# Performance work log

Measured on AMD Instinct MI355X. Metric: run time of the kernel, lower is better.

The kernel has to match this reference:

```python
import jax, jax.numpy as jnp
import numpy as np

DIM = 192
NUM_HEADS = 4
B, H, W = 2, 256, 256
EPS = 1e-12  # torch F.normalize default eps


def setup_inputs() -> dict:
    key = jax.random.key(0)
    k1, k2, k3 = jax.random.split(key, 3)
    x = jax.random.normal(k1, (B, DIM, H, W), dtype=jnp.float32)
    # depthwise qkv conv: groups=DIM, each group maps 1 in-ch -> 3 out-ch; torch OIHW layout (3*DIM, 1, 3, 3)
    w_qkv = jax.random.normal(k2, (3 * DIM, 1, 3, 3), dtype=jnp.float32) * 0.1
    temperature = jnp.ones((NUM_HEADS, 1, 1), dtype=jnp.float32)
    # 1x1 projection conv, stored as [out, in]
    w_proj = jax.random.normal(k3, (DIM, DIM), dtype=jnp.float32) * (1.0 / np.sqrt(DIM))
    return {"x": x, "w_qkv": w_qkv, "temperature": temperature, "w_proj": w_proj}


def reference(x, w_qkv, temperature, w_proj):
    b, c, h, w = x.shape
    num_heads = temperature.shape[0]
    ch = c // num_heads  # channels per head
    # grouped (depthwise) 3x3 conv producing qkv; torch grouped-conv channel order
    # matches feature_group_count ordering (3 consecutive out-chs per group)... but
    # note torch chunk(3, dim=1) splits the 3*c output into contiguous thirds, so
    # q gets out-channels [0, c), etc. We replicate exactly with same layout.
    qkv = jax.lax.conv_general_dilated(
        x, w_qkv, window_strides=(1, 1), padding=((1, 1), (1, 1)),
        feature_group_count=c,
        dimension_numbers=("NCHW", "OIHW", "NCHW"))
    q, k, v = jnp.split(qkv, 3, axis=1)  # each [b, c, h, w]
    q = q.reshape(b, num_heads, ch, h * w)
    k = k.reshape(b, num_heads, ch, h * w)
    v = v.reshape(b, num_heads, ch, h * w)
    # L2 normalize along spatial dim (torch F.normalize with eps clamp)
    q = q / jnp.maximum(jnp.linalg.norm(q, axis=-1, keepdims=True), EPS)
    k = k / jnp.maximum(jnp.linalg.norm(k, axis=-1, keepdims=True), EPS)
    # channel-channel cosine attention, [b, head, ch, ch] (small)
    attn = jnp.einsum("bhcn,bhdn->bhcd", q, k) * temperature
    attn = jax.nn.softmax(attn, axis=-1)
    out = jnp.einsum("bhcd,bhdn->bhcn", attn, v).reshape(b, c, h, w)
    # 1x1 projection conv
    out = jnp.einsum("oi,bihw->bohw", w_proj, out)
    return out
```

## Files before the change

kernel.cpp:

```cpp
#include <hip/hip_runtime.h>
#include <math.h>

#define BB 2
#define CC 192
#define NH 4
#define CH 48
#define SRCP 16
#define HH 256
#define WW 256
#define NPIX (HH*WW)

typedef __attribute__((ext_vector_type(8))) short short8;
typedef __attribute__((ext_vector_type(4))) float f4;

static __device__ __forceinline__ unsigned short f2bf(float f) {
    union { float f; unsigned int u; } c; c.f = f;
    unsigned int r = c.u + 0x7fffu + ((c.u >> 16) & 1u);
    return (unsigned short)(r >> 16);
}

__global__ __launch_bounds__(256, 3) void k_conv(
    const float* __restrict__ x, const float* __restrict__ wqkv,
    unsigned short* __restrict__ vws, float* __restrict__ Sws,
    float* __restrict__ sqws)
{
    __shared__ unsigned int qk32[2][CH][132];

    const int tid = threadIdx.x;
    const int hd = blockIdx.x;
    const int y  = blockIdx.y;
    const int b  = blockIdx.z;

    {
        const int xp = tid;
        const int y0 = (y > 0) ? (y-1) : 0;
        const int y2 = (y < HH-1) ? (y+1) : y;
        const int xl = (xp > 0) ? (xp-1) : 0;
        const int xr = (xp < WW-1) ? (xp+1) : xp;
        const float my0 = (y > 0) ? 1.f : 0.f;
        const float my2 = (y < HH-1) ? 1.f : 0.f;
        const float mx0 = (xp > 0) ? 1.f : 0.f;
        const float mx2 = (xp < WW-1) ? 1.f : 0.f;
        const float m00 = my0*mx0, m02 = my0*mx2, m20 = my2*mx0, m22 = my2*mx2;

        #pragma unroll
        for (int type = 0; type < 2; ++type) {
            const int srcbase = type*64 + SRCP*hd;
            const float* wt = wqkv + type*(CC*9) + hd*(CH*9);
            for (int g4 = 0; g4 < SRCP; g4 += 4) {
                float A[4][9];
                #pragma unroll
                for (int u = 0; u < 4; ++u) {
                    const float* base = x + ((size_t)(b*CC + srcbase + g4 + u)*HH)*WW;
                    const float* r0 = base + (size_t)y0*WW;
                    const float* r1 = base + (size_t)y *WW;
                    const float* r2 = base + (size_t)y2*WW;
                    A[u][0] = r0[xl]; A[u][1] = r0[xp]; A[u][2] = r0[xr];
                    A[u][3] = r1[xl]; A[u][4] = r1[xp]; A[u][5] = r1[xr];
                    A[u][6] = r2[xl]; A[u][7] = r2[xp]; A[u][8] = r2[xr];
                }
                #pragma unroll
                for (int u = 0; u < 4; ++u) {
                    const int g = g4 + u;
                    float a00 = A[u][0]*m00, a01 = A[u][1]*my0, a02 = A[u][2]*m02;
                    float a10 = A[u][3]*mx0, a11 = A[u][4],     a12 = A[u][5]*mx2;
                    float a20 = A[u][6]*m20, a21 = A[u][7]*my2, a22 = A[u][8]*m22;
                    #pragma unroll
                    for (int r = 0; r < 3; ++r) {
                        const int cl = 3*g + r;
                        const float* w = wt + cl*9;
                        float val = a00*w[0] + a01*w[1] + a02*w[2]
                                  + a10*w[3] + a11*w[4] + a12*w[5]
                                  + a20*w[6] + a21*w[7] + a22*w[8];
                        ((unsigned short*)&qk32[type][cl][0])[xp] = f2bf(val);
                    }
                }
            }
        }

        unsigned int vpack[24];
        {
            const int srcbase = 128 + SRCP*hd;
            const float* wt = wqkv + 2*(CC*9) + hd*(CH*9);
            #pragma unroll
            for (int g4 = 0; g4 < SRCP; g4 += 4) {
                float A[4][9];
                #pragma unroll
                for (int u = 0; u < 4; ++u) {
                    const float* base = x + ((size_t)(b*CC + srcbase + g4 + u)*HH)*WW;
                    const float* r0 = base + (size_t)y0*WW;
                    const float* r1 = base + (size_t)y *WW;
                    const float* r2 = base + (size_t)y2*WW;
                    A[u][0] = r0[xl]; A[u][1] = r0[xp]; A[u][2] = r0[xr];
                    A[u][3] = r1[xl]; A[u][4] = r1[xp]; A[u][5] = r1[xr];
                    A[u][6] = r2[xl]; A[u][7] = r2[xp]; A[u][8] = r2[xr];
                }
                #pragma unroll
                for (int u = 0; u < 4; ++u) {
                    const int g = g4 + u;
                    float a00 = A[u][0]*m00, a01 = A[u][1]*my0, a02 = A[u][2]*m02;
                    float a10 = A[u][3]*mx0, a11 = A[u][4],     a12 = A[u][5]*mx2;
                    float a20 = A[u][6]*m20, a21 = A[u][7]*my2, a22 = A[u][8]*m22;
                    #pragma unroll
                    for (int r = 0; r < 3; ++r) {
                        const int cl = 3*g + r;
                        const float* w = wt + cl*9;
                        float val = a00*w[0] + a01*w[1] + a02*w[2]
                                  + a10*w[3] + a11*w[4] + a12*w[5]
                                  + a20*w[6] + a21*w[7] + a22*w[8];
                        unsigned int uu = f2bf(val);
                        if (cl & 1) vpack[cl >> 1] |= (uu << 16);
                        else        vpack[cl >> 1]  = uu;
                    }
                }
            }
        }
        {
            unsigned short* vp = vws + ((size_t)b*NPIX + (size_t)y*WW + xp)*CC + hd*CH;
            #pragma unroll
            for (int st = 0; st < 6; ++st) {
                uint4 u; u.x = vpack[st*4+0]; u.y = vpack[st*4+1];
                         u.z = vpack[st*4+2]; u.w = vpack[st*4+3];
                *(uint4*)(vp + st*8) = u;
            }
        }
    }
    __syncthreads();

    if (tid < 2*CH) {
        const int which = tid / CH;
        const int cl = tid - which*CH;
        const uint4* row = (const uint4*)&qk32[which][cl][0];
        float ssum = 0.f;
        for (int j = 0; j < 32; ++j) {
            uint4 u = row[j];
            #pragma unroll
            for (int q4 = 0; q4 < 4; ++q4) {
                unsigned int w = (&u.x)[q4];
                float lo = __uint_as_float(w << 16);
                float hi = __uint_as_float(w & 0xffff0000u);
                ssum = fmaf(lo, lo, ssum);
                ssum = fmaf(hi, hi, ssum);
            }
        }
        atomicAdd(&sqws[((b*NH + hd)*2 + which)*CH + cl], ssum);
    }

    {
        const int lane = tid & 63;
        const int wv = tid >> 6;
        const int m = lane & 15, quad = lane >> 4;
        for (int p = wv; p < 9; p += 4) {
            const int ct = p / 3, dt = p - ct*3;
            f4 acc = {0.f, 0.f, 0.f, 0.f};
            const char* qbase = (const char*)&qk32[0][ct*16 + m][0] + quad*16;
            const char* kbase = (const char*)&qk32[1][dt*16 + m][0] + quad*16;
            #pragma unroll
            for (int ks = 0; ks < 8; ++ks) {
                short8 afr = *(const short8*)(qbase + ks*64);
                short8 bfr = *(const short8*)(kbase + ks*64);
                acc = __builtin_amdgcn_mfma_f32_16x16x32_bf16(afr, bfr, acc, 0, 0, 0);
            }
            const int c0 = ct*16 + quad*4, d = dt*16 + m;
            float* Sp = Sws + ((size_t)(b*NH + hd)*CH + c0)*CH + d;
            #pragma unroll
            for (int r = 0; r < 4; ++r) atomicAdd(Sp + r*CH, acc[r]);
        }
    }
}

__global__ __launch_bounds__(256) void k_attn(
    const float* __restrict__ Sws, const float* __restrict__ sqws,
    const float* __restrict__ temp, const float* __restrict__ wproj,
    unsigned short* __restrict__ W2bf)
{
    __shared__ float att[CH][CH+1];
    __shared__ float wp[CC][CH+1];
    __shared__ float nrm[2][CH];

    const int tid = threadIdx.x;
    const int b  = blockIdx.x >> 2;
    const int hd = blockIdx.x & 3;

    if (tid < 2*CH) {
        int which = tid / CH, cl = tid - which*CH;
        nrm[which][cl] = fmaxf(sqrtf(sqws[((b*NH + hd)*2 + which)*CH + cl]), 1e-12f);
    }
    __syncthreads();

    const float tscale = temp[hd];
    for (int m = tid; m < CH*CH; m += 256) {
        int c = m / CH, d = m - c*CH;
        att[c][d] = Sws[((size_t)(b*NH + hd)*CH + c)*CH + d] * tscale
                    / (nrm[0][c] * nrm[1][d]);
    }
    __syncthreads();

    if (tid < CH) {
        float mx = -1e30f;
        for (int d = 0; d < CH; ++d) mx = fmaxf(mx, att[tid][d]);
        float sm = 0.f;
        for (int d = 0; d < CH; ++d) { float e = expf(att[tid][d] - mx); att[tid][d] = e; sm += e; }
        float inv = 1.f / sm;
        for (int d = 0; d < CH; ++d) att[tid][d] *= inv;
    }

    for (int m = tid; m < CC*CH; m += 256) {
        int o = m / CH, il = m - o*CH;
        wp[o][il] = wproj[o*CC + hd*CH + il];
    }
    __syncthreads();

    const int o0  = (tid & 31) * 6;
    const int dl0 = (tid >> 5) * 6;
    float a[6][6];
    #pragma unroll
    for (int i = 0; i < 6; ++i)
        #pragma unroll
        for (int j = 0; j < 6; ++j) a[i][j] = 0.f;
    for (int il = 0; il < CH; ++il) {
        float wv[6], av[6];
        #pragma unroll
        for (int i = 0; i < 6; ++i) wv[i] = wp[o0+i][il];
        #pragma unroll
        for (int j = 0; j < 6; ++j) av[j] = att[il][dl0+j];
        #pragma unroll
        for (int i = 0; i < 6; ++i)
            #pragma unroll
            for (int j = 0; j < 6; ++j)
                a[i][j] = fmaf(wv[i], av[j], a[i][j]);
    }
    #pragma unroll
    for (int i = 0; i < 6; ++i)
        #pragma unroll
        for (int j = 0; j < 6; ++j)
            W2bf[((size_t)b*CC + o0 + i)*CC + hd*CH + dl0 + j] = f2bf(a[i][j]);
}

__global__ __launch_bounds__(256, 2) void k_out(
    const unsigned short* __restrict__ vws, const unsigned short* __restrict__ W2bf,
    float* __restrict__ out)
{
    __shared__ unsigned short w2l[CC][200];

    const int tid = threadIdx.x;
    const int b  = blockIdx.y;
    const int n0 = blockIdx.x * 128;

    {
        const uint4* src = (const uint4*)(W2bf + (size_t)b*CC*CC);
        for (int i = tid; i < CC*24; i += 256) {
            int o = i / 24, c = i - o*24;
            *(uint4*)&w2l[o][c*8] = src[i];
        }
    }
    __syncthreads();

    const int lane = tid & 63;
    const int wv = tid >> 6;
    const int m0  = (wv & 1) * 96;
    const int nn0 = (wv >> 1) * 64;
    const int m = lane & 15, quad = lane >> 4;

    f4 acc[6][4];
    #pragma unroll
    for (int mt = 0; mt < 6; ++mt)
        #pragma unroll
        for (int nt = 0; nt < 4; ++nt) acc[mt][nt] = (f4){0.f, 0.f, 0.f, 0.f};

    const unsigned short* vb = vws + ((size_t)b*NPIX + n0 + nn0 + m)*CC + quad*8;

    #pragma unroll
    for (int ks = 0; ks < 6; ++ks) {
        short8 bfr[4];
        #pragma unroll
        for (int nt = 0; nt < 4; ++nt)
            bfr[nt] = *(const short8*)(vb + (size_t)(nt*16)*CC + ks*32);
        short8 afr[6];
        #pragma unroll
        for (int mt = 0; mt < 6; ++mt)
            afr[mt] = *(const short8*)&w2l[m0 + mt*16 + m][ks*32 + quad*8];
        #pragma unroll
        for (int mt = 0; mt < 6; ++mt)
            #pragma unroll
            for (int nt = 0; nt < 4; ++nt)
                acc[mt][nt] = __builtin_amdgcn_mfma_f32_16x16x32_bf16(afr[mt], bfr[nt], acc[mt][nt], 0, 0, 0);
    }

    float* trsp = (float*)w2l;
    const int orow = lane >> 2;
    const int seg  = (lane & 3) * 16;

    #pragma unroll
    for (int ph = 0; ph < 2; ++ph) {
        const int mtb = ph * 3;
        __syncthreads();
        #pragma unroll
        for (int mtl = 0; mtl < 3; ++mtl)
            #pragma unroll
            for (int nt = 0; nt < 4; ++nt)
                #pragma unroll
                for (int r = 0; r < 4; ++r)
                    trsp[((wv*3 + mtl)*16 + quad*4 + r)*68 + nt*16 + m] = acc[mtb+mtl][nt][r];
        __syncthreads();
        #pragma unroll
        for (int mtl = 0; mtl < 3; ++mtl) {
            const float* srcp = &trsp[((wv*3 + mtl)*16 + orow)*68 + seg];
            f4 d0 = *(const f4*)(srcp + 0);
            f4 d1 = *(const f4*)(srcp + 4);
            f4 d2 = *(const f4*)(srcp + 8);
            f4 d3 = *(const f4*)(srcp + 12);
            const int o = m0 + (mtb + mtl)*16 + orow;
            float* op = out + ((size_t)(b*CC + o))*NPIX + n0 + nn0 + seg;
            *(f4*)(op + 0)  = d0;
            *(f4*)(op + 4)  = d1;
            *(f4*)(op + 8)  = d2;
            *(f4*)(op + 12) = d3;
        }
    }
}

extern "C" void kernel_launch(void* const* d_in, const int* in_sizes, int n_in,
                              void* d_out, int out_size, void* d_ws, size_t ws_size,
                              hipStream_t stream)
{
    const float* x     = (const float*)d_in[0];
    const float* wqkv  = (const float*)d_in[1];
    const float* temp  = (const float*)d_in[2];
    const float* wproj = (const float*)d_in[3];
    float* out = (float*)d_out;
    (void)in_sizes; (void)n_in; (void)out_size; (void)ws_size;

    unsigned short* vws = (unsigned short*)d_ws;
    const size_t VBYTES = (size_t)BB*CC*NPIX*sizeof(unsigned short);
    float* Sws  = (float*)((char*)d_ws + VBYTES);
    float* sqws = Sws + (size_t)BB*NH*CH*CH;
    unsigned short* W2bf = (unsigned short*)(sqws + (size_t)BB*NH*2*CH);

    hipMemsetAsync(Sws, 0, (size_t)(BB*NH*CH*CH + BB*NH*2*CH)*sizeof(float), stream);
    k_conv<<<dim3(NH, HH, BB), 256, 0, stream>>>(x, wqkv, vws, Sws, sqws);
    k_attn<<<dim3(BB*NH), 256, 0, stream>>>(Sws, sqws, temp, wproj, W2bf);
    k_out<<<dim3(NPIX/128, BB), 256, 0, stream>>>(vws, W2bf, out);
}
```

Baseline: 313.6 us.

## Split k_out output channels across two blocks to cut LDS and raise occupancy

Each k_out block now handles half of the 192 output channels (96) for a 128-pixel tile, so LDS for the weight tile halves and the accumulator count per wave drops from 24 to 12. Launch bounds go from 2 to 4 blocks per CU and the grid doubles. The transpose staging is reshaped to 32-column rows with phases of 4 and 2 tiles. The cost is that each V tile is now read from global memory twice, once per channel half, which adds traffic in this bandwidth-heavy output stage.

```diff
diff --git a/kernel.cpp b/kernel.cpp
--- a/kernel.cpp
+++ b/kernel.cpp
@@ -237,85 +237,85 @@
             W2bf[((size_t)b*CC + o0 + i)*CC + hd*CH + dl0 + j] = f2bf(a[i][j]);
 }
 
-__global__ __launch_bounds__(256, 2) void k_out(
+__global__ __launch_bounds__(256, 4) void k_out(
     const unsigned short* __restrict__ vws, const unsigned short* __restrict__ W2bf,
     float* __restrict__ out)
 {
-    __shared__ unsigned short w2l[CC][200];
+    __shared__ unsigned short w2l[96][200];
 
     const int tid = threadIdx.x;
-    const int b  = blockIdx.y;
-    const int n0 = blockIdx.x * 128;
+    const int b   = blockIdx.y;
+    const int nblk = blockIdx.x >> 1;
+    const int mh   = blockIdx.x & 1;
+    const int n0 = nblk * 128;
+    const int m_base = mh * 96;
 
     {
-        const uint4* src = (const uint4*)(W2bf + (size_t)b*CC*CC);
-        for (int i = tid; i < CC*24; i += 256) {
+        for (int i = tid; i < 96*24; i += 256) {
             int o = i / 24, c = i - o*24;
-            *(uint4*)&w2l[o][c*8] = src[i];
+            *(uint4*)&w2l[o][c*8] =
+                ((const uint4*)(W2bf + ((size_t)(b*CC + m_base + o))*CC))[c];
         }
     }
     __syncthreads();
 
     const int lane = tid & 63;
     const int wv = tid >> 6;
-    const int m0  = (wv & 1) * 96;
-    const int nn0 = (wv >> 1) * 64;
+    const int nn0 = wv * 32;
     const int m = lane & 15, quad = lane >> 4;
 
-    f4 acc[6][4];
+    f4 acc[6][2];
     #pragma unroll
     for (int mt = 0; mt < 6; ++mt)
         #pragma unroll
-        for (int nt = 0; nt < 4; ++nt) acc[mt][nt] = (f4){0.f, 0.f, 0.f, 0.f};
+        for (int nt = 0; nt < 2; ++nt) acc[mt][nt] = (f4){0.f, 0.f, 0.f, 0.f};
 
     const unsigned short* vb = vws + ((size_t)b*NPIX + n0 + nn0 + m)*CC + quad*8;
 
     #pragma unroll
     for (int ks = 0; ks < 6; ++ks) {
-        short8 bfr[4];
-        #pragma unroll
-        for (int nt = 0; nt < 4; ++nt)
+        short8 bfr[2];
+        #pragma unroll
+        for (int nt = 0; nt < 2; ++nt)
             bfr[nt] = *(const short8*)(vb + (size_t)(nt*16)*CC + ks*32);
-        short8 afr[6];
-        #pragma unroll
-        for (int mt = 0; mt < 6; ++mt)
-            afr[mt] = *(const short8*)&w2l[m0 + mt*16 + m][ks*32 + quad*8];
-        #pragma unroll
-        for (int mt = 0; mt < 6; ++mt)
-            #pragma unroll
-            for (int nt = 0; nt < 4; ++nt)
-                acc[mt][nt] = __builtin_amdgcn_mfma_f32_16x16x32_bf16(afr[mt], bfr[nt], acc[mt][nt], 0, 0, 0);
+        #pragma unroll
+        for (int mt = 0; mt < 6; ++mt) {
+            short8 afr = *(const short8*)&w2l[mt*16 + m][ks*32 + quad*8];
+            #pragma unroll
+            for (int nt = 0; nt < 2; ++nt)
+                acc[mt][nt] = __builtin_amdgcn_mfma_f32_16x16x32_bf16(afr, bfr[nt], acc[mt][nt], 0, 0, 0);
+        }
     }
 
     float* trsp = (float*)w2l;
     const int orow = lane >> 2;
-    const int seg  = (lane & 3) * 16;
+    const int seg  = (lane & 3) * 8;
 
     #pragma unroll
     for (int ph = 0; ph < 2; ++ph) {
-        const int mtb = ph * 3;
+        const int mtb = ph * 4;
+        const int nmt = (ph == 0) ? 4 : 2;
         __syncthreads();
         #pragma unroll
-        for (int mtl = 0; mtl < 3; ++mtl)
-            #pragma unroll
-            for (int nt = 0; nt < 4; ++nt)
+        for (int mtl = 0; mtl < 4; ++mtl) {
+            if (mtl >= nmt) break;
+            #pragma unroll
+            for (int nt = 0; nt < 2; ++nt)
                 #pragma unroll
                 for (int r = 0; r < 4; ++r)
-                    trsp[((wv*3 + mtl)*16 + quad*4 + r)*68 + nt*16 + m] = acc[mtb+mtl][nt][r];
+                    trsp[((wv*4 + mtl)*16 + quad*4 + r)*34 + nt*16 + m] = acc[mtb+mtl][nt][r];
+        }
         __syncthreads();
         #pragma unroll
-        for (int mtl = 0; mtl < 3; ++mtl) {
-            const float* srcp = &trsp[((wv*3 + mtl)*16 + orow)*68 + seg];
+        for (int mtl = 0; mtl < 4; ++mtl) {
+            if (mtl >= nmt) break;
+            const float* srcp = &trsp[((wv*4 + mtl)*16 + orow)*34 + seg];
             f4 d0 = *(const f4*)(srcp + 0);
             f4 d1 = *(const f4*)(srcp + 4);
-            f4 d2 = *(const f4*)(srcp + 8);
-            f4 d3 = *(const f4*)(srcp + 12);
-            const int o = m0 + (mtb + mtl)*16 + orow;
+            const int o = m_base + (mtb + mtl)*16 + orow;
             float* op = out + ((size_t)(b*CC + o))*NPIX + n0 + nn0 + seg;
-            *(f4*)(op + 0)  = d0;
-            *(f4*)(op + 4)  = d1;
-            *(f4*)(op + 8)  = d2;
-            *(f4*)(op + 12) = d3;
+            *(f4*)(op + 0) = d0;
+            *(f4*)(op + 4) = d1;
         }
     }
 }
@@ -340,5 +340,5 @@
     hipMemsetAsync(Sws, 0, (size_t)(BB*NH*CH*CH + BB*NH*2*CH)*sizeof(float), stream);
     k_conv<<<dim3(NH, HH, BB), 256, 0, stream>>>(x, wqkv, vws, Sws, sqws);
     k_attn<<<dim3(BB*NH), 256, 0, stream>>>(Sws, sqws, temp, wproj, W2bf);
-    k_out<<<dim3(NPIX/128, BB), 256, 0, stream>>>(vws, W2bf, out);
-}
+    k_out<<<dim3((NPIX/128)*2, BB), 256, 0, stream>>>(vws, W2bf, out);
+}
```

Result: faster. 298.9 us (-4.7%).
